# Performance work log

Hardware: AMD Instinct MI355X
Metric: run time of the kernel (lower is better)

The kernel has to match this reference:

```python
import jax, jax.numpy as jnp
import numpy as np
from jax import lax

MAX_DECAY = 0.99
EPS = 1e-05
TOPK = 4


def ema_mask_group(moving_avg, new, mask, decay0, cluster_update_num):
    """Faithful port of ema_tensor_mask_group_inplace, including the quirk that
    the Python-level `decay` variable is carried (and possibly shrunk) across
    cluster iterations. Implemented as a lax.scan over clusters carrying decay.
    moving_avg/new: [C] or [C, D]; mask, cluster_update_num: [C].
    """
    def step(decay, xs):
        ma, nw, m, c = xs
        d = jnp.where((m != 0) & (c <= 10.0), decay * c / 10.0, decay)
        out = jnp.where(m != 0, ma * d + nw * (1.0 - d), ma)
        return d, out
    _, out = lax.scan(step, jnp.asarray(decay0, moving_avg.dtype),
                      (moving_avg, new, mask, cluster_update_num))
    return out


def laplace_smoothing(x, n_categories, eps=EPS):
    return (x + eps) / (x.sum() + n_categories * eps)


def setup_inputs() -> dict:
    key = jax.random.key(0)
    k1, k2 = jax.random.split(key)
    N, C, D = 65536, 512, 256
    return {
        "inputs_flatten": jax.random.normal(k1, (N, D), dtype=jnp.float32),
        "dictionary": jax.random.normal(k2, (C, D), dtype=jnp.float32),
        "cluster_size_sum": jnp.zeros((C,), dtype=jnp.float32),
        "cluster_value": jnp.zeros((C, D), dtype=jnp.float32),
        "cluster_update_num": jnp.ones((C,), dtype=jnp.float32),
    }


def reference(inputs_flatten, dictionary, cluster_size_sum, cluster_value,
              cluster_update_num):
    N, D = inputs_flatten.shape
    C = dictionary.shape[0]
    dic = lax.stop_gradient(dictionary)  # dictionary used via .detach()/.data

    # squared euclidean distances [N, C]
    distances = (jnp.sum(inputs_flatten ** 2, axis=1, keepdims=True)
                 + jnp.sum(dic ** 2, axis=1)
                 - 2.0 * jnp.matmul(inputs_flatten, dic.T))

    # ascending sort -> take topK smallest distances
    _, topk_idx = lax.top_k(-distances, TOPK)          # [N, K]
    topk_emb = dic[topk_idx]                            # [N, K, D]
    group_emb = jnp.sum(topk_emb, axis=1) / TOPK        # [N, D]

    # multi-hot encodings via scatter
    rows = jnp.arange(N)[:, None]
    encodings = jnp.zeros((N, C), dtype=jnp.float32).at[rows, topk_idx].set(1.0)

    # ---- training-mode EMA codebook update (single device: all_gather = identity) ----
    x_sg = lax.stop_gradient(inputs_flatten)
    cluster_size = jnp.sum(encodings, axis=0)           # [C]
    cluster_mask = (cluster_size != 0).astype(jnp.float32)
    cluster_update_num_new = cluster_update_num + cluster_mask

    cluster_size_sum_new = ema_mask_group(cluster_size_sum, cluster_size,
                                          cluster_mask, MAX_DECAY,
                                          cluster_update_num_new)
    input_sum = jnp.matmul(encodings.T, x_sg)           # [C, D]
    cluster_value_new = ema_mask_group(cluster_value, input_sum, cluster_mask,
                                       MAX_DECAY, cluster_update_num_new)

    cs = laplace_smoothing(cluster_size_sum_new, C, EPS) * cluster_size_sum_new.sum()
    embed_normalized = jnp.where(cluster_mask[:, None] == 1.0,
                                 cluster_value_new / cs[:, None],
                                 cluster_value_new)
    dictionary_new = embed_normalized                   # world_size == 1

    # straight-through estimator
    group_emb = lax.stop_gradient(group_emb - inputs_flatten) + inputs_flatten
    return (group_emb, topk_idx, dictionary_new, cluster_size_sum_new,
            cluster_value_new, cluster_update_num_new)
```

## Files before the change

### kernel.cpp

```cpp
#include <hip/hip_runtime.h>

#define N_ROWS 65536
#define C_CLUST 512
#define D_DIM 256

#define WS_DICTT   0
#define WS_DSQ     131072
#define WS_XSQ     131584
#define WS_CS      197120
#define WS_DCY     197632
#define WS_ISUM    198144
#define WS_COUNTS  329216
#define WS_OFFSETS 329728
#define WS_FILL    330752
#define WS_ROWLIST 331264

#define OUT_GEMB 0
#define OUT_TOPK 16777216
#define OUT_DICT 17039360
#define OUT_CSS  17170432
#define OUT_CV   17170944
#define OUT_CNUM 17302016

#define RPB 128

typedef __attribute__((ext_vector_type(8))) short short8;
typedef __attribute__((ext_vector_type(16))) float f32x16;

__device__ __forceinline__ unsigned short f2bf(float v) {
    union { float f; unsigned u; } c; c.f = v;
    unsigned r = c.u + 0x7FFFu + ((c.u >> 16) & 1u);
    return (unsigned short)(r >> 16);
}
__device__ __forceinline__ float bf2f(unsigned short h) {
    union { float f; unsigned u; } c; c.u = ((unsigned)h) << 16;
    return c.f;
}

__global__ void zero_k(unsigned* counts, unsigned* fill, float* isum) {
    int t = blockIdx.x * blockDim.x + threadIdx.x;
    if (t < 512) { counts[t] = 0u; fill[t] = 0u; }
    if (t < C_CLUST * D_DIM) isum[t] = 0.f;
}

__global__ void prep_dict(const float* __restrict__ dic, float* __restrict__ ws) {
    int c = blockIdx.x, k = threadIdx.x;
    float v = dic[c * D_DIM + k];
    unsigned short* dhi = (unsigned short*)(ws + WS_DICTT);
    unsigned short* dlo = dhi + 131072;
    unsigned short hb = f2bf(v);
    dhi[c * D_DIM + k] = hb;
    dlo[c * D_DIM + k] = f2bf(__fsub_rn(v, bf2f(hb)));
    __shared__ float red[256];
    red[k] = v * v;
    __syncthreads();
    for (int s = 128; s > 0; s >>= 1) {
        if (k < s) red[k] += red[k + s];
        __syncthreads();
    }
    if (k == 0) ws[WS_DSQ + c] = red[0];
}

__global__ void row_sq(const float* __restrict__ x, float* __restrict__ ws) {
    int row = blockIdx.x, k = threadIdx.x;
    float v = x[row * D_DIM + k];
    __shared__ float red[256];
    red[k] = v * v;
    __syncthreads();
    for (int s = 128; s > 0; s >>= 1) {
        if (k < s) red[k] += red[k + s];
        __syncthreads();
    }
    if (k == 0) ws[WS_XSQ + row] = red[0];
}

__global__ __launch_bounds__(256, 2) void stage1_cand(
    const float* __restrict__ x, const float* __restrict__ ws,
    float* __restrict__ cand_out)
{
    __shared__ unsigned short hlds[32 * 264];
    __shared__ unsigned short llds[32 * 264];
    __shared__ float dsq_s[512];

    const int tid = threadIdx.x;
    const int lane = tid & 63;
    const int w = tid >> 6;
    const int kg = lane >> 5;
    const int cl_lane = lane & 31;
    const int row = blockIdx.x * 128 + w * 32 + cl_lane;

    const unsigned short* dhi = (const unsigned short*)(ws + WS_DICTT);
    const unsigned short* dlo = dhi + 131072;

    for (int i = tid; i < 512; i += 256) dsq_s[i] = ws[WS_DSQ + i];

    short8 bhi[16], blo[16];
    #pragma unroll
    for (int s = 0; s < 16; ++s) {
        const float* px = &x[(size_t)row * D_DIM + s * 16 + kg * 8];
        float4 u0 = *reinterpret_cast<const float4*>(px);
        float4 u1 = *reinterpret_cast<const float4*>(px + 4);
        float vv[8] = {u0.x, u0.y, u0.z, u0.w, u1.x, u1.y, u1.z, u1.w};
        short8 h, l;
        #pragma unroll
        for (int e = 0; e < 8; ++e) {
            unsigned short hb = f2bf(vv[e]);
            unsigned short lb = f2bf(__fsub_rn(vv[e], bf2f(hb)));
            h[e] = (short)hb; l[e] = (short)lb;
        }
        bhi[s] = h; blo[s] = l;
    }

    unsigned long long kk[8];
    #pragma unroll
    for (int q = 0; q < 8; ++q) kk[q] = 0xFFFFFFFFFFFFFFFFULL;

    for (int ct = 0; ct < 16; ++ct) {
        __syncthreads();
        for (int q = tid; q < 1024; q += 256) {
            int c = q >> 5, k8 = (q & 31) * 8;
            *reinterpret_cast<uint4*>(&hlds[c * 264 + k8]) =
                *reinterpret_cast<const uint4*>(&dhi[(ct * 32 + c) * D_DIM + k8]);
            *reinterpret_cast<uint4*>(&llds[c * 264 + k8]) =
                *reinterpret_cast<const uint4*>(&dlo[(ct * 32 + c) * D_DIM + k8]);
        }
        __syncthreads();

        f32x16 ahh, ahl, alh;
        #pragma unroll
        for (int r = 0; r < 16; ++r) { ahh[r] = 0.f; ahl[r] = 0.f; alh[r] = 0.f; }

        #pragma unroll
        for (int s = 0; s < 16; ++s) {
            short8 Ah = *reinterpret_cast<const short8*>(
                &hlds[cl_lane * 264 + s * 16 + kg * 8]);
            short8 Al = *reinterpret_cast<const short8*>(
                &llds[cl_lane * 264 + s * 16 + kg * 8]);
            ahh = __builtin_amdgcn_mfma_f32_32x32x16_bf16(Ah, bhi[s], ahh, 0, 0, 0);
            ahl = __builtin_amdgcn_mfma_f32_32x32x16_bf16(Ah, blo[s], ahl, 0, 0, 0);
            alh = __builtin_amdgcn_mfma_f32_32x32x16_bf16(Al, bhi[s], alh, 0, 0, 0);
        }

        #pragma unroll
        for (int r = 0; r < 16; ++r) {
            int cl = ct * 32 + (r & 3) + 8 * (r >> 2) + 4 * kg;
            float dot = ahh[r] + ahl[r] + alh[r];
            float key = (dsq_s[cl] + 1024.0f) - 2.0f * dot;
            unsigned long long v =
                ((unsigned long long)__float_as_uint(key) << 32) | (unsigned)cl;
            #pragma unroll
            for (int q = 0; q < 8; ++q) {
                bool lt = v < kk[q];
                unsigned long long mn = lt ? v : kk[q];
                unsigned long long mx = lt ? kk[q] : v;
                kk[q] = mn; v = mx;
            }
        }
    }

    uint4 wv;
    wv.x = (unsigned)(kk[0] & 0xFFFF) | ((unsigned)(kk[1] & 0xFFFF) << 16);
    wv.y = (unsigned)(kk[2] & 0xFFFF) | ((unsigned)(kk[3] & 0xFFFF) << 16);
    wv.z = (unsigned)(kk[4] & 0xFFFF) | ((unsigned)(kk[5] & 0xFFFF) << 16);
    wv.w = (unsigned)(kk[6] & 0xFFFF) | ((unsigned)(kk[7] & 0xFFFF) << 16);
    *reinterpret_cast<uint4*>(&cand_out[(size_t)row * 256 + kg * 4]) = wv;
}

__global__ __launch_bounds__(256, 4) void refine_k(
    const float* __restrict__ x, const float* __restrict__ dic,
    const float* __restrict__ ws, float* __restrict__ out,
    unsigned* __restrict__ counts)
{
    __shared__ float xl[16 * 260];
    __shared__ float dstage[256 * 17];
    __shared__ float distb[256];
    __shared__ int cidx[256];

    const int t = threadIdx.x;
    const int rowBase = blockIdx.x * 16;
    const unsigned short* candp = (const unsigned short*)(out + OUT_GEMB);

    cidx[t] = (int)candp[(size_t)(rowBase + (t >> 4)) * 512 + (t & 15)];

    #pragma unroll
    for (int i = 0; i < 4; ++i) {
        int q = t + i * 256;
        int r = q >> 6, seg = q & 63;
        *reinterpret_cast<float4*>(&xl[r * 260 + seg * 4]) =
            *reinterpret_cast<const float4*>(
                &x[(size_t)(rowBase + r) * D_DIM + seg * 4]);
    }
    __syncthreads();

    const float* dbase[4];
    int spair[4], sf4[4];
    #pragma unroll
    for (int i = 0; i < 4; ++i) {
        int q = t + i * 256;
        spair[i] = q >> 2;
        sf4[i] = q & 3;
        dbase[i] = &dic[(size_t)cidx[spair[i]] * D_DIM + sf4[i] * 4];
    }

    const int r = t >> 4;
    const float* xp = &xl[r * 260];
    float acc = 0.f;

    for (int chunk = 0; chunk < 16; ++chunk) {
        #pragma unroll
        for (int i = 0; i < 4; ++i) {
            float4 dv = *reinterpret_cast<const float4*>(dbase[i] + chunk * 16);
            float* dst = &dstage[spair[i] * 17 + sf4[i] * 4];
            dst[0] = dv.x; dst[1] = dv.y; dst[2] = dv.z; dst[3] = dv.w;
        }
        __syncthreads();
        const float* dp = &dstage[t * 17];
        const float* xc = xp + chunk * 16;
        #pragma unroll
        for (int k = 0; k < 16; ++k)
            acc = fmaf(xc[k], dp[k], acc);
        __syncthreads();
    }

    {
        int ci = cidx[t];
        float ds = ws[WS_DSQ + ci];
        float xs = ws[WS_XSQ + rowBase + r];
        distb[t] = __fsub_rn(__fadd_rn(xs, ds), __fmul_rn(2.0f, acc));
    }
    __syncthreads();

    if (t < 16) {
        float bv0 = 3.4e38f, bv1 = 3.4e38f, bv2 = 3.4e38f, bv3 = 3.4e38f;
        int bi0 = 0x7FFFFFFF, bi1 = 0x7FFFFFFF, bi2 = 0x7FFFFFFF, bi3 = 0x7FFFFFFF;
        for (int s = 0; s < 16; ++s) {
            int p = t * 16 + s;
            float v = distb[p];
            int ci = cidx[p];
            if (v < bv3 || (v == bv3 && ci < bi3)) {
                if (v < bv2 || (v == bv2 && ci < bi2)) {
                    bv3 = bv2; bi3 = bi2;
                    if (v < bv1 || (v == bv1 && ci < bi1)) {
                        bv2 = bv1; bi2 = bi1;
                        if (v < bv0 || (v == bv0 && ci < bi0)) {
                            bv1 = bv0; bi1 = bi0;
                            bv0 = v; bi0 = ci;
                        } else { bv1 = v; bi1 = ci; }
                    } else { bv2 = v; bi2 = ci; }
                } else { bv3 = v; bi3 = ci; }
            }
        }
        int row = rowBase + t;
        out[OUT_TOPK + (size_t)row * 4 + 0] = (float)bi0;
        out[OUT_TOPK + (size_t)row * 4 + 1] = (float)bi1;
        out[OUT_TOPK + (size_t)row * 4 + 2] = (float)bi2;
        out[OUT_TOPK + (size_t)row * 4 + 3] = (float)bi3;
        atomicAdd(&counts[bi0], 1u);
        atomicAdd(&counts[bi1], 1u);
        atomicAdd(&counts[bi2], 1u);
        atomicAdd(&counts[bi3], 1u);
    }
}

__global__ __launch_bounds__(256, 4) void group_emb_k(
    const float* __restrict__ x, const float* __restrict__ dic,
    const float* __restrict__ topk, float* __restrict__ out)
{
    const int t = threadIdx.x;
    const int row = blockIdx.x * 4 + (t >> 6);
    const int k4 = (t & 63) * 4;
    int i0 = (int)topk[(size_t)row * 4 + 0];
    int i1 = (int)topk[(size_t)row * 4 + 1];
    int i2 = (int)topk[(size_t)row * 4 + 2];
    int i3 = (int)topk[(size_t)row * 4 + 3];
    float4 a = *reinterpret_cast<const float4*>(&dic[(size_t)i0 * D_DIM + k4]);
    float4 b = *reinterpret_cast<const float4*>(&dic[(size_t)i1 * D_DIM + k4]);
    float4 c = *reinterpret_cast<const float4*>(&dic[(size_t)i2 * D_DIM + k4]);
    float4 e = *reinterpret_cast<const float4*>(&dic[(size_t)i3 * D_DIM + k4]);
    float4 xv = *reinterpret_cast<const float4*>(&x[(size_t)row * D_DIM + k4]);
    float4 o;
    float g;
    g = __fmul_rn(__fadd_rn(__fadd_rn(__fadd_rn(a.x, b.x), c.x), e.x), 0.25f);
    o.x = __fadd_rn(__fsub_rn(g, xv.x), xv.x);
    g = __fmul_rn(__fadd_rn(__fadd_rn(__fadd_rn(a.y, b.y), c.y), e.y), 0.25f);
    o.y = __fadd_rn(__fsub_rn(g, xv.y), xv.y);
    g = __fmul_rn(__fadd_rn(__fadd_rn(__fadd_rn(a.z, b.z), c.z), e.z), 0.25f);
    o.z = __fadd_rn(__fsub_rn(g, xv.z), xv.z);
    g = __fmul_rn(__fadd_rn(__fadd_rn(__fadd_rn(a.w, b.w), c.w), e.w), 0.25f);
    o.w = __fadd_rn(__fsub_rn(g, xv.w), xv.w);
    *reinterpret_cast<float4*>(&out[OUT_GEMB + (size_t)row * D_DIM + k4]) = o;
}

__global__ void prefix_k(const unsigned* __restrict__ counts, unsigned* __restrict__ offsets) {
    __shared__ unsigned s[512];
    int t = threadIdx.x;
    unsigned my = counts[t];
    s[t] = my;
    __syncthreads();
    for (int off = 1; off < 512; off <<= 1) {
        unsigned v = (t >= off) ? s[t - off] : 0u;
        __syncthreads();
        s[t] += v;
        __syncthreads();
    }
    offsets[t] = s[t] - my;
    if (t == 511) offsets[512] = s[511];
}

__global__ void scatter_k(const float* __restrict__ topk, const unsigned* __restrict__ offsets,
                          unsigned* __restrict__ fill, unsigned* __restrict__ rowlist) {
    int row = blockIdx.x * 256 + threadIdx.x;
    #pragma unroll
    for (int k = 0; k < 4; ++k) {
        int c = (int)topk[row * 4 + k];
        unsigned p = atomicAdd(&fill[c], 1u);
        rowlist[offsets[c] + p] = ((unsigned)c << 16) | (unsigned)row;
    }
}

__global__ __launch_bounds__(256, 8) void cluster_sum2_k(
    const float* __restrict__ x, const unsigned* __restrict__ rowlist,
    float* __restrict__ isum)
{
    const int d = threadIdx.x;
    const int base = blockIdx.x * RPB;
    unsigned e0 = rowlist[base];
    int ccur = (int)(e0 >> 16);
    float acc = 0.f;
    #pragma unroll 4
    for (int j = 0; j < RPB; ++j) {
        unsigned e = rowlist[base + j];
        int c = (int)(e >> 16);
        float v = x[(e & 0xFFFFu) * D_DIM + d];
        if (c != ccur) {
            atomicAdd(&isum[ccur * D_DIM + d], acc);
            acc = 0.f;
            ccur = c;
        }
        acc += v;
    }
    atomicAdd(&isum[ccur * D_DIM + d], acc);
}

__global__ void ema_scalar_k(const float* __restrict__ css_in, const float* __restrict__ cnum_in,
                             const unsigned* __restrict__ counts,
                             float* __restrict__ ws, float* __restrict__ out) {
    __shared__ float sdecay[512];
    __shared__ float sred[512];
    __shared__ float scn[512];
    __shared__ unsigned smask[512];
    int t = threadIdx.x;
    unsigned cnt = counts[t];
    float size = (float)cnt;
    float mask = (cnt != 0u) ? 1.f : 0.f;
    float cnum_new = __fadd_rn(cnum_in[t], mask);
    scn[t] = cnum_new;
    smask[t] = cnt;
    __syncthreads();
    if (t == 0) {
        float d = 0.99f;
        for (int c = 0; c < 512; ++c) {
            if (smask[c] != 0u && scn[c] <= 10.0f)
                d = __fmul_rn(d, scn[c]) / 10.0f;
            sdecay[c] = d;
        }
    }
    __syncthreads();
    float d = sdecay[t];
    float css = css_in[t];
    float css_new = (cnt != 0u)
        ? __fadd_rn(__fmul_rn(css, d), __fmul_rn(size, __fsub_rn(1.f, d)))
        : css;
    out[OUT_CSS + t] = css_new;
    out[OUT_CNUM + t] = cnum_new;
    sred[t] = css_new;
    __syncthreads();
    for (int s = 256; s > 0; s >>= 1) {
        if (t < s) sred[t] += sred[t + s];
        __syncthreads();
    }
    float S = sred[0];
    float cs = __fmul_rn(__fdiv_rn(__fadd_rn(css_new, 1e-5f),
                                   __fadd_rn(S, 0.00512f)), S);
    ws[WS_CS + t] = cs;
    ws[WS_DCY + t] = d;
}

__global__ void final_k(const float* __restrict__ cv_in, const float* __restrict__ ws,
                        const unsigned* __restrict__ counts, float* __restrict__ out) {
    int c = blockIdx.x, d = threadIdx.x;
    float isum = ws[WS_ISUM + c * D_DIM + d];
    float dc = ws[WS_DCY + c];
    float cs = ws[WS_CS + c];
    unsigned cnt = counts[c];
    float cv = cv_in[c * D_DIM + d];
    float cvn = (cnt != 0u)
        ? __fadd_rn(__fmul_rn(cv, dc), __fmul_rn(isum, __fsub_rn(1.f, dc)))
        : cv;
    out[OUT_CV + c * D_DIM + d] = cvn;
    out[OUT_DICT + c * D_DIM + d] = (cnt != 0u) ? __fdiv_rn(cvn, cs) : cvn;
}

extern "C" void kernel_launch(void* const* d_in, const int* in_sizes, int n_in,
                              void* d_out, int out_size, void* d_ws, size_t ws_size,
                              hipStream_t stream) {
    const float* x       = (const float*)d_in[0];
    const float* dic     = (const float*)d_in[1];
    const float* css_in  = (const float*)d_in[2];
    const float* cv_in   = (const float*)d_in[3];
    const float* cnum_in = (const float*)d_in[4];
    float* out = (float*)d_out;
    float* ws  = (float*)d_ws;
    unsigned* counts  = (unsigned*)(ws + WS_COUNTS);
    unsigned* offsets = (unsigned*)(ws + WS_OFFSETS);
    unsigned* fill    = (unsigned*)(ws + WS_FILL);
    unsigned* rowlist = (unsigned*)(ws + WS_ROWLIST);

    zero_k<<<C_CLUST * D_DIM / 256, 256, 0, stream>>>(counts, fill, ws + WS_ISUM);
    prep_dict<<<C_CLUST, 256, 0, stream>>>(dic, ws);
    row_sq<<<N_ROWS, 256, 0, stream>>>(x, ws);

    stage1_cand<<<N_ROWS / 128, 256, 0, stream>>>(x, ws, out + OUT_GEMB);

    refine_k<<<N_ROWS / 16, 256, 0, stream>>>(x, dic, ws, out, counts);
    group_emb_k<<<N_ROWS / 4, 256, 0, stream>>>(x, dic, out + OUT_TOPK, out + OUT_GEMB);

    prefix_k<<<1, 512, 0, stream>>>(counts, offsets);
    scatter_k<<<N_ROWS / 256, 256, 0, stream>>>(out + OUT_TOPK, offsets, fill, rowlist);
    cluster_sum2_k<<<N_ROWS * 4 / RPB, 256, 0, stream>>>(x, rowlist, ws + WS_ISUM);
    ema_scalar_k<<<1, 512, 0, stream>>>(css_in, cnum_in, counts, ws, out);
    final_k<<<C_CLUST, 256, 0, stream>>>(cv_in, ws, counts, out);
}
```

Before: 651.1 us.

## Stream transposed dictionary through LDS in refine instead of gathering candidate rows

prep_dict now also writes a transposed fp32 copy of the dictionary into workspace, reusing the rowlist region before scatter_k needs it. refine_k now handles 64 rows per block and streams the whole transposed dictionary through LDS in 16-dimension chunks, with register double-buffered prefetch. Each thread then computes exact dot products for its 4 candidates by indexing LDS by cluster id. This replaces uncoalesced per-candidate global gathers with coalesced streaming and cuts total L2 traffic. The cost is random-index LDS reads that may cause bank conflicts, plus larger LDS use.

```diff
diff --git a/kernel.cpp b/kernel.cpp
--- a/kernel.cpp
+++ b/kernel.cpp
@@ -51,6 +51,7 @@
     unsigned short hb = f2bf(v);
     dhi[c * D_DIM + k] = hb;
     dlo[c * D_DIM + k] = f2bf(__fsub_rn(v, bf2f(hb)));
+    ws[WS_ROWLIST + k * C_CLUST + c] = v;
     __shared__ float red[256];
     red[k] = v * v;
     __syncthreads();
@@ -167,70 +168,91 @@
 }
 
 __global__ __launch_bounds__(256, 4) void refine_k(
-    const float* __restrict__ x, const float* __restrict__ dic,
-    const float* __restrict__ ws, float* __restrict__ out,
-    unsigned* __restrict__ counts)
+    const float* __restrict__ x, const float* __restrict__ ws,
+    float* __restrict__ out, unsigned* __restrict__ counts)
 {
-    __shared__ float xl[16 * 260];
-    __shared__ float dstage[256 * 17];
-    __shared__ float distb[256];
-    __shared__ int cidx[256];
+    __shared__ float dlds[16 * 516];
+    __shared__ float xlds[16 * 68];
+    __shared__ int   cidx[1024];
+    __shared__ float distb[1024];
 
     const int t = threadIdx.x;
-    const int rowBase = blockIdx.x * 16;
+    const int rowBase = blockIdx.x * 64;
+    const float* dictT = ws + WS_ROWLIST;
     const unsigned short* candp = (const unsigned short*)(out + OUT_GEMB);
-
-    cidx[t] = (int)candp[(size_t)(rowBase + (t >> 4)) * 512 + (t & 15)];
 
     #pragma unroll
     for (int i = 0; i < 4; ++i) {
         int q = t + i * 256;
-        int r = q >> 6, seg = q & 63;
-        *reinterpret_cast<float4*>(&xl[r * 260 + seg * 4]) =
-            *reinterpret_cast<const float4*>(
-                &x[(size_t)(rowBase + r) * D_DIM + seg * 4]);
-    }
-    __syncthreads();
-
-    const float* dbase[4];
-    int spair[4], sf4[4];
+        cidx[q] = (int)candp[(size_t)(rowBase + (q >> 4)) * 512 + (q & 15)];
+    }
+    __syncthreads();
+
+    const int rl = t >> 2;
+    const int sb = (t & 3) * 4;
+    const int c0 = cidx[rl * 16 + sb + 0];
+    const int c1 = cidx[rl * 16 + sb + 1];
+    const int c2 = cidx[rl * 16 + sb + 2];
+    const int c3 = cidx[rl * 16 + sb + 3];
+
+    float4 dreg[8];
+    float4 xreg;
     #pragma unroll
-    for (int i = 0; i < 4; ++i) {
-        int q = t + i * 256;
-        spair[i] = q >> 2;
-        sf4[i] = q & 3;
-        dbase[i] = &dic[(size_t)cidx[spair[i]] * D_DIM + sf4[i] * 4];
-    }
-
-    const int r = t >> 4;
-    const float* xp = &xl[r * 260];
-    float acc = 0.f;
-
-    for (int chunk = 0; chunk < 16; ++chunk) {
-        #pragma unroll
-        for (int i = 0; i < 4; ++i) {
-            float4 dv = *reinterpret_cast<const float4*>(dbase[i] + chunk * 16);
-            float* dst = &dstage[spair[i] * 17 + sf4[i] * 4];
-            dst[0] = dv.x; dst[1] = dv.y; dst[2] = dv.z; dst[3] = dv.w;
-        }
-        __syncthreads();
-        const float* dp = &dstage[t * 17];
-        const float* xc = xp + chunk * 16;
-        #pragma unroll
-        for (int k = 0; k < 16; ++k)
-            acc = fmaf(xc[k], dp[k], acc);
+    for (int i = 0; i < 8; ++i)
+        dreg[i] = *reinterpret_cast<const float4*>(&dictT[(size_t)(t + i * 256) * 4]);
+    xreg = *reinterpret_cast<const float4*>(
+        &x[(size_t)(rowBase + (t >> 2)) * D_DIM + (t & 3) * 4]);
+
+    float a0 = 0.f, a1 = 0.f, a2 = 0.f, a3 = 0.f;
+
+    for (int c = 0; c < 16; ++c) {
+        #pragma unroll
+        for (int i = 0; i < 8; ++i) {
+            int g = t + i * 256;
+            *reinterpret_cast<float4*>(&dlds[(g >> 7) * 516 + (g & 127) * 4]) = dreg[i];
+        }
+        {
+            int f4 = t & 3, r = t >> 2;
+            xlds[(f4 * 4 + 0) * 68 + r] = xreg.x;
+            xlds[(f4 * 4 + 1) * 68 + r] = xreg.y;
+            xlds[(f4 * 4 + 2) * 68 + r] = xreg.z;
+            xlds[(f4 * 4 + 3) * 68 + r] = xreg.w;
+        }
+        if (c < 15) {
+            #pragma unroll
+            for (int i = 0; i < 8; ++i)
+                dreg[i] = *reinterpret_cast<const float4*>(
+                    &dictT[(size_t)((c + 1) * 2048 + t + i * 256) * 4]);
+            xreg = *reinterpret_cast<const float4*>(
+                &x[(size_t)(rowBase + (t >> 2)) * D_DIM + (c + 1) * 16 + (t & 3) * 4]);
+        }
+        __syncthreads();
+        #pragma unroll
+        for (int kk = 0; kk < 16; ++kk) {
+            float xv = xlds[kk * 68 + rl];
+            const float* dr = &dlds[kk * 516];
+            a0 = fmaf(xv, dr[c0], a0);
+            a1 = fmaf(xv, dr[c1], a1);
+            a2 = fmaf(xv, dr[c2], a2);
+            a3 = fmaf(xv, dr[c3], a3);
+        }
         __syncthreads();
     }
 
     {
-        int ci = cidx[t];
-        float ds = ws[WS_DSQ + ci];
-        float xs = ws[WS_XSQ + rowBase + r];
-        distb[t] = __fsub_rn(__fadd_rn(xs, ds), __fmul_rn(2.0f, acc));
-    }
-    __syncthreads();
-
-    if (t < 16) {
+        float xs = ws[WS_XSQ + rowBase + rl];
+        distb[rl * 16 + sb + 0] =
+            __fsub_rn(__fadd_rn(xs, ws[WS_DSQ + c0]), __fmul_rn(2.0f, a0));
+        distb[rl * 16 + sb + 1] =
+            __fsub_rn(__fadd_rn(xs, ws[WS_DSQ + c1]), __fmul_rn(2.0f, a1));
+        distb[rl * 16 + sb + 2] =
+            __fsub_rn(__fadd_rn(xs, ws[WS_DSQ + c2]), __fmul_rn(2.0f, a2));
+        distb[rl * 16 + sb + 3] =
+            __fsub_rn(__fadd_rn(xs, ws[WS_DSQ + c3]), __fmul_rn(2.0f, a3));
+    }
+    __syncthreads();
+
+    if (t < 64) {
         float bv0 = 3.4e38f, bv1 = 3.4e38f, bv2 = 3.4e38f, bv3 = 3.4e38f;
         int bi0 = 0x7FFFFFFF, bi1 = 0x7FFFFFFF, bi2 = 0x7FFFFFFF, bi3 = 0x7FFFFFFF;
         for (int s = 0; s < 16; ++s) {
@@ -422,7 +444,7 @@
 
     stage1_cand<<<N_ROWS / 128, 256, 0, stream>>>(x, ws, out + OUT_GEMB);
 
-    refine_k<<<N_ROWS / 16, 256, 0, stream>>>(x, dic, ws, out, counts);
+    refine_k<<<N_ROWS / 64, 256, 0, stream>>>(x, ws, out, counts);
     group_emb_k<<<N_ROWS / 4, 256, 0, stream>>>(x, dic, out + OUT_TOPK, out + OUT_GEMB);
 
     prefix_k<<<1, 512, 0, stream>>>(counts, offsets);
```

Result: slower. 682.6 us (+4.8%).
